# Kernel tuning notes

Hardware: AMD Instinct MI355X
Metric: run time of the kernel (lower is better)

The kernel has to match this reference:

```python
import jax, jax.numpy as jnp
import numpy as np

HID, NHEAD, NLAYERS = 128, 8, 6
BS, H, W = 1, 64, 128
HD = HID // NHEAD  # head dim = 16


def layer_norm(x, g, b, eps=1e-5):
    m = jnp.mean(x, -1, keepdims=True)
    v = jnp.mean((x - m) ** 2, -1, keepdims=True)
    return (x - m) * jax.lax.rsqrt(v + eps) * g + b


def mha_relative(query, kv, in_w, in_b, out_w, out_b, pos_enc, pos_idx, attn_mask, is_self):
    # query/kv: [W, N, C]; in_w: [3C, C]; pos_enc: [2W-1, C]; pos_idx: [W*W]
    w, n, c = query.shape
    if is_self:
        q, k, v = jnp.split(query @ in_w.T + in_b, 3, axis=-1)
    else:
        q = query @ in_w[:c].T + in_b[:c]
        k, v = jnp.split(kv @ in_w[c:].T + in_b[c:], 2, axis=-1)
    # relative positional bias: gather [2W-1,C] -> [W,W,C], project with q/k weights
    pos_sel = pos_enc[pos_idx].reshape(w, w, c)
    q_r, k_r = jnp.split(pos_sel @ in_w[:2 * c].T + in_b[:2 * c], 2, axis=-1)
    scale = HD ** -0.5
    q = (q * scale).reshape(w, n, NHEAD, HD)
    k = k.reshape(w, n, NHEAD, HD)
    v = v.reshape(w, n, NHEAD, HD)
    q_r = (q_r * scale).reshape(w, w, NHEAD, HD)
    k_r = k_r.reshape(w, w, NHEAD, HD)
    attn = (jnp.einsum('wnec,vnec->newv', q, k)
            + jnp.einsum('wnec,wvec->newv', q, k_r)
            + jnp.einsum('vnec,wvec->newv', k, q_r))  # [N,E,W,W]
    if attn_mask is not None:
        attn = attn + attn_mask[None, None]
    raw_attn = attn.sum(axis=1)  # [N,W,W] head-summed raw scores
    a = jax.nn.softmax(attn, axis=-1)
    v_o = jnp.einsum('newv,vnec->wnec', a, v).reshape(w, n, c)
    return v_o @ out_w.T + out_b, raw_attn


def setup_inputs() -> dict:
    key = jax.random.key(0)
    ks = jax.random.split(key, 8)
    f32 = jnp.float32
    s = 0.02
    d = {}
    d['feat_left'] = jax.random.normal(ks[0], (BS, HID, H, W), f32)
    d['feat_right'] = jax.random.normal(ks[1], (BS, HID, H, W), f32)
    d['pos_enc'] = jax.random.normal(ks[2], (2 * W - 1, HID), f32)
    d['self_ln_g'] = jnp.ones((NLAYERS, HID), f32)
    d['self_ln_b'] = jnp.zeros((NLAYERS, HID), f32)
    d['self_in_w'] = jax.random.normal(ks[3], (NLAYERS, 3 * HID, HID), f32) * s
    d['self_in_b'] = jnp.zeros((NLAYERS, 3 * HID), f32)
    d['self_out_w'] = jax.random.normal(ks[4], (NLAYERS, HID, HID), f32) * s
    d['self_out_b'] = jnp.zeros((NLAYERS, HID), f32)
    d['cross_ln1_g'] = jnp.ones((NLAYERS, HID), f32)
    d['cross_ln1_b'] = jnp.zeros((NLAYERS, HID), f32)
    d['cross_ln2_g'] = jnp.ones((NLAYERS, HID), f32)
    d['cross_ln2_b'] = jnp.zeros((NLAYERS, HID), f32)
    d['cross_in_w'] = jax.random.normal(ks[5], (NLAYERS, 3 * HID, HID), f32) * s
    d['cross_in_b'] = jnp.zeros((NLAYERS, 3 * HID), f32)
    d['cross_out_w'] = jax.random.normal(ks[6], (NLAYERS, HID, HID), f32) * s
    d['cross_out_b'] = jnp.zeros((NLAYERS, HID), f32)
    return d


def reference(feat_left, feat_right, pos_enc, self_ln_g, self_ln_b, self_in_w, self_in_b,
              self_out_w, self_out_b, cross_ln1_g, cross_ln1_b, cross_ln2_g, cross_ln2_b,
              cross_in_w, cross_in_b, cross_out_w, cross_out_b):
    bs, c, hn, w = feat_left.shape  # bs must be 1 (as in source)
    # [N,C,H,W] -> [W, H*N, C]
    fl = jnp.transpose(feat_left, (3, 2, 0, 1)).reshape(w, hn * bs, c)
    fr = jnp.transpose(feat_right, (3, 2, 0, 1)).reshape(w, hn * bs, c)
    HN = hn * bs
    # pos_indexes[i,j] = (w-1-i) + j, values in [0, 2w-2]
    pos_idx = ((w - 1 - jnp.arange(w))[:, None] + jnp.arange(w)[None, :]).reshape(-1)
    causal = jnp.triu(jnp.full((w, w), -jnp.inf, feat_left.dtype), k=1)
    feat = jnp.concatenate([fl, fr], axis=1)  # [W, 2HN, C]
    raw_attn = None
    for i in range(NLAYERS):
        # self attention over concatenated left+right rows
        f2 = layer_norm(feat, self_ln_g[i], self_ln_b[i])
        upd, _ = mha_relative(f2, f2, self_in_w[i], self_in_b[i], self_out_w[i],
                              self_out_b[i], pos_enc, pos_idx, None, True)
        feat = feat + upd
        left, right = feat[:, :HN], feat[:, HN:]
        # cross attention: left queries attend to norm2(right)
        # (source computes a right-update with norm1/flipped pos but discards it)
        l2 = layer_norm(left, cross_ln1_g[i], cross_ln1_b[i])
        r2 = layer_norm(right, cross_ln2_g[i], cross_ln2_b[i])
        mask = causal if i == NLAYERS - 1 else None
        upd, raw_attn = mha_relative(l2, r2, cross_in_w[i], cross_in_b[i], cross_out_w[i],
                                     cross_out_b[i], pos_enc, pos_idx, mask, False)
        left = left + upd
        feat = jnp.concatenate([left, right], axis=1)
    # [HN,W,W] -> [bs, hn, W, W]
    return jnp.transpose(raw_attn.reshape(hn, bs, w, w), (1, 0, 2, 3))
```

## Files before the change

kernel.cpp:

```cpp
#include <hip/hip_runtime.h>
#include <cmath>

#define CDIM 128

typedef __attribute__((ext_vector_type(8))) short bf16x8;
typedef __attribute__((ext_vector_type(4))) float f32x4;
typedef unsigned short u16;

__device__ inline unsigned pk2(float a, float b) {
    unsigned ua = __float_as_uint(a) + 0x8000u;
    unsigned ub = __float_as_uint(b) + 0x8000u;
    return (ua >> 16) | (ub & 0xffff0000u);
}
__device__ inline u16 pk1(float x) {
    return (u16)((__float_as_uint(x) + 0x8000u) >> 16);
}
__device__ inline float ubf(u16 u) { return __uint_as_float(((unsigned)u) << 16); }
__device__ inline float ulo(unsigned u) { return __uint_as_float(u << 16); }
__device__ inline float uhi(unsigned u) { return __uint_as_float(u & 0xffff0000u); }

__global__ __launch_bounds__(256) void init_feat_kernel(const float* __restrict__ FL,
                                                        const float* __restrict__ FR,
                                                        u16* __restrict__ feat) {
    __shared__ float t[32][33];
    int cb = blockIdx.x, wb = blockIdx.y, n = blockIdx.z;
    const float* src = (n < 64) ? FL : FR;
    int nn = n & 63;
    int j = threadIdx.x & 31, i0 = threadIdx.x >> 5;
    #pragma unroll
    for (int p = 0; p < 4; p++) {
        int i = i0 + p * 8;
        t[i][j] = src[(cb * 32 + i) * 8192 + nn * 128 + wb * 32 + j];
    }
    __syncthreads();
    #pragma unroll
    for (int p = 0; p < 4; p++) {
        int i = i0 + p * 8;
        feat[((long)(wb * 32 + i) * 128 + n) * 128 + cb * 32 + j] = pk1(t[j][i]);
    }
}

__global__ __launch_bounds__(256) void convert_w_kernel(const float* __restrict__ w0,
                                                        const float* __restrict__ w1,
                                                        const float* __restrict__ w2,
                                                        const float* __restrict__ w3,
                                                        const float* __restrict__ b0,
                                                        const float* __restrict__ b1,
                                                        u16* __restrict__ wout,
                                                        float* __restrict__ bout) {
    int idx = blockIdx.x * 256 + threadIdx.x;
    if (idx < 196608) {
        const float* src; long off4; u16* dst;
        if (idx < 73728)       { src = w0; off4 = idx;           dst = wout; }
        else if (idx < 147456) { src = w1; off4 = idx - 73728;   dst = wout + 294912; }
        else if (idx < 172032) { src = w2; off4 = idx - 147456;  dst = wout + 589824; }
        else                   { src = w3; off4 = idx - 172032;  dst = wout + 688128; }
        float4 f = *(const float4*)(src + off4 * 4);
        *(uint2*)(dst + off4 * 4) = make_uint2(pk2(f.x, f.y), pk2(f.z, f.w));
    } else {
        int t = idx - 196608;
        if (t < 4608) bout[t] = (t < 2304) ? b0[t] : b1[t - 2304];
    }
}

__global__ __launch_bounds__(256) void ln0_kernel(const u16* __restrict__ feat,
                                                  const float* __restrict__ g,
                                                  const float* __restrict__ b,
                                                  u16* __restrict__ lnB) {
    int tid = threadIdx.x, wv = tid >> 6, lane = tid & 63;
    float g0 = g[lane * 2], b0 = b[lane * 2];
    float g1 = g[lane * 2 + 1], b1 = b[lane * 2 + 1];
    #pragma unroll
    for (int rr = 0; rr < 4; rr++) {
        long m = (long)blockIdx.x * 16 + wv * 4 + rr;
        unsigned u = *(const unsigned*)(feat + m * 128 + lane * 2);
        float x0 = ulo(u), x1 = uhi(u);
        float s = x0 + x1, q = x0 * x0 + x1 * x1;
        #pragma unroll
        for (int off = 1; off < 64; off <<= 1) {
            s += __shfl_xor(s, off);
            q += __shfl_xor(q, off);
        }
        float mean = s * (1.f / 128.f);
        float var = q * (1.f / 128.f) - mean * mean;
        float rs = rsqrtf(var + 1e-5f);
        float y0 = (x0 - mean) * rs * g0 + b0;
        float y1 = (x1 - mean) * rs * g1 + b1;
        *(unsigned*)(lnB + m * 128 + lane * 2) = pk2(y0, y1);
    }
}

__global__ __launch_bounds__(256, 4) void gemm_pp_kernel(const float* __restrict__ A,
                                                         const u16* __restrict__ W,
                                                         const float* __restrict__ bias,
                                                         u16* __restrict__ C,
                                                         int M, int N, int ldc,
                                                         float scale,
                                                         int wz, int bz, int cz) {
    __shared__ __align__(16) u16 sA[64 * 136];
    __shared__ __align__(16) u16 sW[64 * 136];
    int z = blockIdx.z;
    W += (long)z * wz;
    bias += z * bz;
    C += (long)z * cz;
    int tid = threadIdx.x;
    int row0 = blockIdx.y * 64, col0 = blockIdx.x * 64;
    float4 zf4 = make_float4(0.f, 0.f, 0.f, 0.f);
    int kc = tid & 31;
    #pragma unroll
    for (int i = 0; i < 8; i++) {
        int r = (tid + i * 256) >> 5;
        int m = row0 + r;
        int jn = col0 + r;
        float4 fa = (m < M) ? *(const float4*)(A + (long)m * 128 + kc * 4) : zf4;
        uint2 uw = make_uint2(0u, 0u);
        if (jn < N) uw = *(const uint2*)(W + (long)jn * 128 + kc * 4);
        *(uint2*)&sA[r * 136 + kc * 4] = make_uint2(pk2(fa.x, fa.y), pk2(fa.z, fa.w));
        *(uint2*)&sW[r * 136 + kc * 4] = uw;
    }
    __syncthreads();

    int wv = tid >> 6, lane = tid & 63, quad = lane >> 4, col = lane & 15;
    f32x4 z4 = {0.f, 0.f, 0.f, 0.f};
    f32x4 acc0 = z4, acc1 = z4, acc2 = z4, acc3 = z4;
    #pragma unroll
    for (int kb = 0; kb < 4; kb++) {
        bf16x8 a = *(const bf16x8*)&sA[(wv * 16 + col) * 136 + kb * 32 + quad * 8];
        bf16x8 b0 = *(const bf16x8*)&sW[(0 * 16 + col) * 136 + kb * 32 + quad * 8];
        bf16x8 b1 = *(const bf16x8*)&sW[(1 * 16 + col) * 136 + kb * 32 + quad * 8];
        bf16x8 b2 = *(const bf16x8*)&sW[(2 * 16 + col) * 136 + kb * 32 + quad * 8];
        bf16x8 b3 = *(const bf16x8*)&sW[(3 * 16 + col) * 136 + kb * 32 + quad * 8];
        acc0 = __builtin_amdgcn_mfma_f32_16x16x32_bf16(a, b0, acc0, 0, 0, 0);
        acc1 = __builtin_amdgcn_mfma_f32_16x16x32_bf16(a, b1, acc1, 0, 0, 0);
        acc2 = __builtin_amdgcn_mfma_f32_16x16x32_bf16(a, b2, acc2, 0, 0, 0);
        acc3 = __builtin_amdgcn_mfma_f32_16x16x32_bf16(a, b3, acc3, 0, 0, 0);
    }
    int mrow = row0 + wv * 16 + quad * 4;
    #pragma unroll
    for (int tc = 0; tc < 4; tc++) {
        f32x4 acc = tc == 0 ? acc0 : tc == 1 ? acc1 : tc == 2 ? acc2 : acc3;
        int jn = col0 + tc * 16 + col;
        if (jn >= N) continue;
        float bs = bias[jn];
        float sc = (jn < 128) ? scale : 1.f;
        #pragma unroll
        for (int reg = 0; reg < 4; reg++) {
            int m = mrow + reg;
            if (m >= M) continue;
            C[(long)m * ldc + jn] = pk1((acc[reg] + bs) * sc);
        }
    }
}

__global__ __launch_bounds__(256, 3) void gemm_qkv128_kernel(const u16* __restrict__ A,
                                                             const u16* __restrict__ W,
                                                             const float* __restrict__ bias,
                                                             u16* __restrict__ C,
                                                             float scale) {
    __shared__ __align__(16) u16 sA[128 * 136];
    __shared__ __align__(16) u16 sW[64 * 136];
    int tid = threadIdx.x;
    int row0 = blockIdx.y * 128, col0 = blockIdx.x * 64;
    int kc = tid & 31;
    #pragma unroll
    for (int i = 0; i < 16; i++) {
        int r = (tid + i * 256) >> 5;
        *(uint2*)&sA[r * 136 + kc * 4] =
            *(const uint2*)(A + (long)(row0 + r) * 128 + kc * 4);
    }
    #pragma unroll
    for (int i = 0; i < 8; i++) {
        int r = (tid + i * 256) >> 5;
        *(uint2*)&sW[r * 136 + kc * 4] =
            *(const uint2*)(W + (long)(col0 + r) * 128 + kc * 4);
    }
    __syncthreads();

    int wv = tid >> 6, lane = tid & 63, quad = lane >> 4, col = lane & 15;
    f32x4 z4 = {0.f, 0.f, 0.f, 0.f};
    f32x4 accA0 = z4, accA1 = z4, accA2 = z4, accA3 = z4;
    f32x4 accB0 = z4, accB1 = z4, accB2 = z4, accB3 = z4;
    #pragma unroll
    for (int kb = 0; kb < 4; kb++) {
        bf16x8 a0 = *(const bf16x8*)&sA[(wv * 32 + col) * 136 + kb * 32 + quad * 8];
        bf16x8 a1 = *(const bf16x8*)&sA[(wv * 32 + 16 + col) * 136 + kb * 32 + quad * 8];
        bf16x8 b0 = *(const bf16x8*)&sW[(0 * 16 + col) * 136 + kb * 32 + quad * 8];
        bf16x8 b1 = *(const bf16x8*)&sW[(1 * 16 + col) * 136 + kb * 32 + quad * 8];
        bf16x8 b2 = *(const bf16x8*)&sW[(2 * 16 + col) * 136 + kb * 32 + quad * 8];
        bf16x8 b3 = *(const bf16x8*)&sW[(3 * 16 + col) * 136 + kb * 32 + quad * 8];
        accA0 = __builtin_amdgcn_mfma_f32_16x16x32_bf16(a0, b0, accA0, 0, 0, 0);
        accA1 = __builtin_amdgcn_mfma_f32_16x16x32_bf16(a0, b1, accA1, 0, 0, 0);
        accA2 = __builtin_amdgcn_mfma_f32_16x16x32_bf16(a0, b2, accA2, 0, 0, 0);
        accA3 = __builtin_amdgcn_mfma_f32_16x16x32_bf16(a0, b3, accA3, 0, 0, 0);
        accB0 = __builtin_amdgcn_mfma_f32_16x16x32_bf16(a1, b0, accB0, 0, 0, 0);
        accB1 = __builtin_amdgcn_mfma_f32_16x16x32_bf16(a1, b1, accB1, 0, 0, 0);
        accB2 = __builtin_amdgcn_mfma_f32_16x16x32_bf16(a1, b2, accB2, 0, 0, 0);
        accB3 = __builtin_amdgcn_mfma_f32_16x16x32_bf16(a1, b3, accB3, 0, 0, 0);
    }
    #pragma unroll
    for (int st = 0; st < 2; st++) {
        int mrow = row0 + wv * 32 + st * 16 + quad * 4;
        #pragma unroll
        for (int tc = 0; tc < 4; tc++) {
            f32x4 acc;
            if (st == 0) acc = tc == 0 ? accA0 : tc == 1 ? accA1 : tc == 2 ? accA2 : accA3;
            else         acc = tc == 0 ? accB0 : tc == 1 ? accB1 : tc == 2 ? accB2 : accB3;
            int jn = col0 + tc * 16 + col;
            float bs = bias[jn];
            float sc = (jn < 128) ? scale : 1.f;
            #pragma unroll
            for (int reg = 0; reg < 4; reg++)
                C[(long)(mrow + reg) * 384 + jn] = pk1((acc[reg] + bs) * sc);
        }
    }
}

__global__ __launch_bounds__(256, 3) void gemm_out_self_kernel(const u16* __restrict__ A,
                                                               const u16* __restrict__ W,
                                                               const float* __restrict__ bias,
                                                               u16* __restrict__ feat,
                                                               const float* __restrict__ g1,
                                                               const float* __restrict__ b1,
                                                               const float* __restrict__ g2,
                                                               const float* __restrict__ b2,
                                                               u16* __restrict__ lnA,
                                                               const float* __restrict__ sng,
                                                               const float* __restrict__ snb,
                                                               u16* __restrict__ lnB) {
    __shared__ __align__(16) u16 sA[64 * 136];
    __shared__ __align__(16) u16 sW[128 * 136];
    int tid = threadIdx.x;
    int by = blockIdx.x;
    int row0 = by * 64;
    int kc = tid & 31;
    #pragma unroll
    for (int i = 0; i < 8; i++) {
        int r = (tid + i * 256) >> 5;
        *(uint2*)&sA[r * 136 + kc * 4] = *(const uint2*)(A + (long)(row0 + r) * 128 + kc * 4);
    }
    #pragma unroll
    for (int i = 0; i < 16; i++) {
        int r = (tid + i * 256) >> 5;
        *(uint2*)&sW[r * 136 + kc * 4] = *(const uint2*)(W + (long)r * 128 + kc * 4);
    }
    __syncthreads();

    int wv = tid >> 6, lane = tid & 63, quad = lane >> 4, col = lane & 15;
    f32x4 acc[8] = {};
    #pragma unroll
    for (int kb = 0; kb < 4; kb++) {
        bf16x8 a = *(const bf16x8*)&sA[(wv * 16 + col) * 136 + kb * 32 + quad * 8];
        #pragma unroll
        for (int tc = 0; tc < 8; tc++) {
            bf16x8 b = *(const bf16x8*)&sW[(tc * 16 + col) * 136 + kb * 32 + quad * 8];
            acc[tc] = __builtin_amdgcn_mfma_f32_16x16x32_bf16(a, b, acc[tc], 0, 0, 0);
        }
    }
    int right = by & 1;
    const float* gA = right ? g2 : g1;
    const float* bA = right ? b2 : b1;
    float gAv[8], bAv[8], gBv[8], bBv[8], bsv[8];
    bool doB = (sng != nullptr) && right;
    #pragma unroll
    for (int tc = 0; tc < 8; tc++) {
        int jn = tc * 16 + col;
        gAv[tc] = gA[jn]; bAv[tc] = bA[jn]; bsv[tc] = bias[jn];
        if (doB) { gBv[tc] = sng[jn]; bBv[tc] = snb[jn]; }
    }
    #pragma unroll
    for (int reg = 0; reg < 4; reg++) {
        long m = row0 + wv * 16 + quad * 4 + reg;
        long rb = m * 128;
        float o[8];
        float s = 0.f, q = 0.f;
        #pragma unroll
        for (int tc = 0; tc < 8; tc++) {
            int jn = tc * 16 + col;
            float v = acc[tc][reg] + bsv[tc] + ubf(feat[rb + jn]);
            o[tc] = v; s += v; q += v * v;
        }
        #pragma unroll
        for (int off = 1; off < 16; off <<= 1) {
            s += __shfl_xor(s, off);
            q += __shfl_xor(q, off);
        }
        float mean = s * (1.f / 128.f);
        float var = q * (1.f / 128.f) - mean * mean;
        float rs = rsqrtf(var + 1e-5f);
        #pragma unroll
        for (int tc = 0; tc < 8; tc++) {
            int jn = tc * 16 + col;
            feat[rb + jn] = pk1(o[tc]);
            float ln = (o[tc] - mean) * rs;
            lnA[rb + jn] = pk1(ln * gAv[tc] + bAv[tc]);
            if (doB) lnB[rb + jn] = pk1(ln * gBv[tc] + bBv[tc]);
        }
    }
}

__global__ __launch_bounds__(256, 3) void gemm_out_cross_kernel(const u16* __restrict__ A,
                                                                const u16* __restrict__ W,
                                                                const float* __restrict__ bias,
                                                                u16* __restrict__ feat,
                                                                const float* __restrict__ sng,
                                                                const float* __restrict__ snb,
                                                                u16* __restrict__ lnB) {
    __shared__ __align__(16) u16 sA[64 * 136];
    __shared__ __align__(16) u16 sW[128 * 136];
    int tid = threadIdx.x;
    int row0 = blockIdx.x * 64;
    int kc = tid & 31;
    #pragma unroll
    for (int i = 0; i < 8; i++) {
        int r = (tid + i * 256) >> 5;
        *(uint2*)&sA[r * 136 + kc * 4] = *(const uint2*)(A + (long)(row0 + r) * 128 + kc * 4);
    }
    #pragma unroll
    for (int i = 0; i < 16; i++) {
        int r = (tid + i * 256) >> 5;
        *(uint2*)&sW[r * 136 + kc * 4] = *(const uint2*)(W + (long)r * 128 + kc * 4);
    }
    __syncthreads();

    int wv = tid >> 6, lane = tid & 63, quad = lane >> 4, col = lane & 15;
    f32x4 acc[8] = {};
    #pragma unroll
    for (int kb = 0; kb < 4; kb++) {
        bf16x8 a = *(const bf16x8*)&sA[(wv * 16 + col) * 136 + kb * 32 + quad * 8];
        #pragma unroll
        for (int tc = 0; tc < 8; tc++) {
            bf16x8 b = *(const bf16x8*)&sW[(tc * 16 + col) * 136 + kb * 32 + quad * 8];
            acc[tc] = __builtin_amdgcn_mfma_f32_16x16x32_bf16(a, b, acc[tc], 0, 0, 0);
        }
    }
    float gBv[8], bBv[8], bsv[8];
    #pragma unroll
    for (int tc = 0; tc < 8; tc++) {
        int jn = tc * 16 + col;
        gBv[tc] = sng[jn]; bBv[tc] = snb[jn]; bsv[tc] = bias[jn];
    }
    #pragma unroll
    for (int reg = 0; reg < 4; reg++) {
        long m = row0 + wv * 16 + quad * 4 + reg;
        long rb = ((m >> 6) * 128 + (m & 63)) * 128;
        float o[8];
        float s = 0.f, q = 0.f;
        #pragma unroll
        for (int tc = 0; tc < 8; tc++) {
            int jn = tc * 16 + col;
            float v = acc[tc][reg] + bsv[tc] + ubf(feat[rb + jn]);
            o[tc] = v; s += v; q += v * v;
        }
        #pragma unroll
        for (int off = 1; off < 16; off <<= 1) {
            s += __shfl_xor(s, off);
            q += __shfl_xor(q, off);
        }
        float mean = s * (1.f / 128.f);
        float var = q * (1.f / 128.f) - mean * mean;
        float rs = rsqrtf(var + 1e-5f);
        #pragma unroll
        for (int tc = 0; tc < 8; tc++) {
            int jn = tc * 16 + col;
            feat[rb + jn] = pk1(o[tc]);
            lnB[rb + jn] = pk1((o[tc] - mean) * rs * gBv[tc] + bBv[tc]);
        }
    }
}

__global__ __launch_bounds__(256, 4) void gemm_cross_qkv_kernel(const u16* __restrict__ lnA,
                                                                const u16* __restrict__ Wq,
                                                                const float* __restrict__ biasq,
                                                                u16* __restrict__ qout,
                                                                u16* __restrict__ kvout,
                                                                float scale) {
    int bx = blockIdx.x;
    int z = (bx >= 2) ? 1 : 0;
    int cx = z ? bx - 2 : bx;
    const u16* W     = z ? Wq + 16384 : Wq;
    const float* bia = z ? biasq + 128 : biasq;
    u16* C           = z ? kvout : qout;
    int N   = z ? 256 : 128;
    int ldc = N;
    int n_off = z ? 64 : 0;
    float sc  = z ? 1.f : scale;

    __shared__ __align__(16) u16 sA[64 * 136];
    __shared__ __align__(16) u16 sW[64 * 136];
    int tid = threadIdx.x;
    int row0 = blockIdx.y * 64, col0 = cx * 64;
    int kc = tid & 31;
    #pragma unroll
    for (int i = 0; i < 8; i++) {
        int r = (tid + i * 256) >> 5;
        int m = row0 + r;
        int jn = col0 + r;
        long xr = (long)((m >> 6) * 128 + (m & 63) + n_off);
        uint2 uw = make_uint2(0u, 0u);
        if (jn < N) uw = *(const uint2*)(W + (long)jn * 128 + kc * 4);
        *(uint2*)&sA[r * 136 + kc * 4] = *(const uint2*)(lnA + xr * 128 + kc * 4);
        *(uint2*)&sW[r * 136 + kc * 4] = uw;
    }
    __syncthreads();

    int wv = tid >> 6, lane = tid & 63, quad = lane >> 4, col = lane & 15;
    f32x4 z4 = {0.f, 0.f, 0.f, 0.f};
    f32x4 acc0 = z4, acc1 = z4, acc2 = z4, acc3 = z4;
    #pragma unroll
    for (int kb = 0; kb < 4; kb++) {
        bf16x8 a = *(const bf16x8*)&sA[(wv * 16 + col) * 136 + kb * 32 + quad * 8];
        bf16x8 b0 = *(const bf16x8*)&sW[(0 * 16 + col) * 136 + kb * 32 + quad * 8];
        bf16x8 b1 = *(const bf16x8*)&sW[(1 * 16 + col) * 136 + kb * 32 + quad * 8];
        bf16x8 b2 = *(const bf16x8*)&sW[(2 * 16 + col) * 136 + kb * 32 + quad * 8];
        bf16x8 b3 = *(const bf16x8*)&sW[(3 * 16 + col) * 136 + kb * 32 + quad * 8];
        acc0 = __builtin_amdgcn_mfma_f32_16x16x32_bf16(a, b0, acc0, 0, 0, 0);
        acc1 = __builtin_amdgcn_mfma_f32_16x16x32_bf16(a, b1, acc1, 0, 0, 0);
        acc2 = __builtin_amdgcn_mfma_f32_16x16x32_bf16(a, b2, acc2, 0, 0, 0);
        acc3 = __builtin_amdgcn_mfma_f32_16x16x32_bf16(a, b3, acc3, 0, 0, 0);
    }
    int mrow = row0 + wv * 16 + quad * 4;
    #pragma unroll
    for (int tc = 0; tc < 4; tc++) {
        f32x4 acc = tc == 0 ? acc0 : tc == 1 ? acc1 : tc == 2 ? acc2 : acc3;
        int jn = col0 + tc * 16 + col;
        if (jn >= N) continue;
        float bs = bia[jn];
        #pragma unroll
        for (int reg = 0; reg < 4; reg++) {
            int m = mrow + reg;
            C[(long)m * ldc + jn] = pk1((acc[reg] + bs) * sc);
        }
    }
}

__global__ __launch_bounds__(512, 6) void attn_kernel(const u16* __restrict__ Q, int qs,
                                                      const u16* __restrict__ K, int ks,
                                                      const u16* __restrict__ V, int vs,
                                                      const u16* __restrict__ PP,
                                                      u16* __restrict__ VO,
                                                      float* __restrict__ RAW,
                                                      int NN, int causal) {
    __shared__ __align__(16) u16 sm[26624];
    const int SK = 0, R2 = 3072, SA = 9216;
    int e = blockIdx.x, n = blockIdx.y;
    int tid = threadIdx.x;
    int wv = tid >> 6, lane = tid & 63, quad = lane >> 4, col = lane & 15;

    bf16x8 zf = {0, 0, 0, 0, 0, 0, 0, 0};
    f32x4 z4 = {0.f, 0.f, 0.f, 0.f};
    bf16x8 aQ = zf, aK = zf;
    if (quad < 2) {
        aQ = *(const bf16x8*)(Q + (long)((wv * 16 + col) * NN + n) * qs + e * 16 + quad * 8);
        aK = *(const bf16x8*)(K + (long)((wv * 16 + col) * NN + n) * ks + e * 16 + quad * 8);
    }
    {
        int row = tid >> 2, c = tid & 3;
        *(uint2*)&sm[SK + row * 24 + c * 4] =
            *(const uint2*)(K + (long)(row * NN + n) * ks + e * 16 + c * 4);
    }
    for (int t = tid; t < 1024; t += 512) {
        int r = t >> 2, c = t & 3;
        uint2 uk = make_uint2(0u, 0u);
        if (r < 255) uk = *(const uint2*)(PP + r * 256 + 128 + e * 16 + c * 4);
        *(uint2*)&sm[R2 + r * 24 + c * 4] = uk;
    }
    __syncthreads();

    f32x4 s1[8];
    #pragma unroll
    for (int tv = 0; tv < 8; tv++) {
        bf16x8 b = zf;
        if (quad < 2) b = *(const bf16x8*)&sm[SK + (tv * 16 + col) * 24 + quad * 8];
        s1[tv] = __builtin_amdgcn_mfma_f32_16x16x32_bf16(aQ, b, z4, 0, 0, 0);
    }
    int wbq = wv * 16 + quad * 4;
    int s2lo = 7 - wv;
    for (int tt = 0; tt < 9; tt++) {
        int tr = s2lo + tt;
        bf16x8 b = zf;
        if (quad < 2) b = *(const bf16x8*)&sm[R2 + (tr * 16 + col) * 24 + quad * 8];
        f32x4 d = __builtin_amdgcn_mfma_f32_16x16x32_bf16(aQ, b, z4, 0, 0, 0);
        #pragma unroll
        for (int reg = 0; reg < 4; reg++) {
            int v = tr * 16 + col - 127 + wbq + reg;
            if (v >= 0 && v < 128) sm[SA + (wbq + reg) * 136 + v] = pk1(d[reg]);
        }
    }
    __syncthreads();
    for (int t = tid; t < 1024; t += 512) {
        int r = t >> 2, c = t & 3;
        uint2 uq = make_uint2(0u, 0u);
        if (r < 255) uq = *(const uint2*)(PP + r * 256 + e * 16 + c * 4);
        *(uint2*)&sm[R2 + r * 24 + c * 4] = uq;
    }
    {
        int row = tid >> 2, c = tid & 3;
        uint2 uv = *(const uint2*)(V + (long)(row * NN + n) * vs + e * 16 + c * 4);
        sm[SK + (c * 4 + 0) * 136 + row] = (u16)(uv.x & 0xffffu);
        sm[SK + (c * 4 + 1) * 136 + row] = (u16)(uv.x >> 16);
        sm[SK + (c * 4 + 2) * 136 + row] = (u16)(uv.y & 0xffffu);
        sm[SK + (c * 4 + 3) * 136 + row] = (u16)(uv.y >> 16);
    }
    __syncthreads();
    for (int tt = 0; tt < 9; tt++) {
        int tr = wv + tt;
        bf16x8 b = zf;
        if (quad < 2) b = *(const bf16x8*)&sm[R2 + (tr * 16 + col) * 24 + quad * 8];
        f32x4 d = __builtin_amdgcn_mfma_f32_16x16x32_bf16(aK, b, z4, 0, 0, 0);
        #pragma unroll
        for (int reg = 0; reg < 4; reg++) {
            int v = wbq + reg;
            int w = 127 + v - (tr * 16 + col);
            if (w >= 0 && w < 128) {
                int addr = SA + w * 136 + v;
                sm[addr] = pk1(ubf(sm[addr]) + d[reg]);
            }
        }
    }
    __syncthreads();

    float rs0 = 0.f, rs1 = 0.f, rs2 = 0.f, rs3 = 0.f;
    #pragma unroll
    for (int tv = 0; tv < 8; tv++) {
        f32x4 c = s1[tv];
        int v = tv * 16 + col;
        #pragma unroll
        for (int reg = 0; reg < 4; reg++) {
            int w = wbq + reg;
            int addr = SA + w * 136 + v;
            float a = c[reg] + ubf(sm[addr]);
            bool live = !(causal && v > w);
            float p = live ? __expf(a) : 0.f;
            if (RAW) RAW[(long)n * 16384 + w * 128 + v] = live ? a : 0.f;
            sm[addr] = pk1(p);
            if (reg == 0) rs0 += p; else if (reg == 1) rs1 += p;
            else if (reg == 2) rs2 += p; else rs3 += p;
        }
    }
    #pragma unroll
    for (int o = 1; o < 16; o <<= 1) {
        rs0 += __shfl_xor(rs0, o);
        rs1 += __shfl_xor(rs1, o);
        rs2 += __shfl_xor(rs2, o);
        rs3 += __shfl_xor(rs3, o);
    }
    __syncthreads();

    f32x4 o4 = z4;
    #pragma unroll
    for (int kb = 0; kb < 4; kb++) {
        bf16x8 a = *(const bf16x8*)&sm[SA + (wv * 16 + col) * 136 + kb * 32 + quad * 8];
        bf16x8 b = *(const bf16x8*)&sm[SK + col * 136 + kb * 32 + quad * 8];
        o4 = __builtin_amdgcn_mfma_f32_16x16x32_bf16(a, b, o4, 0, 0, 0);
    }
    float iv0 = 1.f / rs0, iv1 = 1.f / rs1, iv2 = 1.f / rs2, iv3 = 1.f / rs3;
    VO[(long)((wbq + 0) * NN + n) * CDIM + e * 16 + col] = pk1(o4[0] * iv0);
    VO[(long)((wbq + 1) * NN + n) * CDIM + e * 16 + col] = pk1(o4[1] * iv1);
    VO[(long)((wbq + 2) * NN + n) * CDIM + e * 16 + col] = pk1(o4[2] * iv2);
    VO[(long)((wbq + 3) * NN + n) * CDIM + e * 16 + col] = pk1(o4[3] * iv3);
}

extern "C" void kernel_launch(void* const* d_in, const int* in_sizes, int n_in,
                              void* d_out, int out_size, void* d_ws, size_t ws_size,
                              hipStream_t stream) {
    const float* FL         = (const float*)d_in[0];
    const float* FR         = (const float*)d_in[1];
    const float* pos_enc    = (const float*)d_in[2];
    const float* self_ln_g  = (const float*)d_in[3];
    const float* self_ln_b  = (const float*)d_in[4];
    const float* self_in_w  = (const float*)d_in[5];
    const float* self_in_b  = (const float*)d_in[6];
    const float* self_out_w = (const float*)d_in[7];
    const float* self_out_b = (const float*)d_in[8];
    const float* cr_ln1_g   = (const float*)d_in[9];
    const float* cr_ln1_b   = (const float*)d_in[10];
    const float* cr_ln2_g   = (const float*)d_in[11];
    const float* cr_ln2_b   = (const float*)d_in[12];
    const float* cr_in_w    = (const float*)d_in[13];
    const float* cr_in_b    = (const float*)d_in[14];
    const float* cr_out_w   = (const float*)d_in[15];
    const float* cr_out_b   = (const float*)d_in[16];

    float* ws       = (float*)d_ws;
    u16*   feat     = (u16*)ws;
    u16*   vo       = (u16*)(ws + 1048576);
    u16*   qkv      = (u16*)(ws + 2097152);
    u16*   kvx      = qkv + 3145728;
    u16*   pp_self  = (u16*)(ws + 5242880);
    u16*   pp_cross = pp_self + 391680;
    u16*   wbf      = (u16*)(ws + 5634560);
    u16*   wsel_in  = wbf;
    u16*   wcr_in   = wbf + 294912;
    u16*   wsel_out = wbf + 589824;
    u16*   wcr_out  = wbf + 688128;
    float* bin      = ws + 6027776;
    u16*   lnA      = (u16*)(ws + 6032384);
    u16*   lnB      = (u16*)(ws + 7080960);
    float* out      = (float*)d_out;

    const float scale = 0.25f;

    convert_w_kernel<<<786, 256, 0, stream>>>(self_in_w, cr_in_w, self_out_w, cr_out_w,
                                              self_in_b, cr_in_b, wbf, bin);
    init_feat_kernel<<<dim3(4, 4, 128), 256, 0, stream>>>(FL, FR, feat);
    ln0_kernel<<<1024, 256, 0, stream>>>(feat, self_ln_g, self_ln_b, lnB);
    gemm_pp_kernel<<<dim3(4, 4, 12), 256, 0, stream>>>(pos_enc, wsel_in, bin, pp_self,
                                                       255, 256, 256, scale,
                                                       49152, 384, 65280);

    for (int i = 0; i < 6; i++) {
        int last = (i == 5);
        gemm_qkv128_kernel<<<dim3(6, 128), 256, 0, stream>>>(lnB, wsel_in + i * 49152,
                                                             self_in_b + i * 384, qkv, scale);
        attn_kernel<<<dim3(8, 128), 512, 0, stream>>>(qkv, 384, qkv + 128, 384, qkv + 256, 384,
                                                      pp_self + i * 65280, vo, nullptr, 128, 0);
        gemm_out_self_kernel<<<256, 256, 0, stream>>>(vo, wsel_out + i * 16384,
                                                      self_out_b + i * 128, feat,
                                                      cr_ln1_g + i * 128, cr_ln1_b + i * 128,
                                                      cr_ln2_g + i * 128, cr_ln2_b + i * 128,
                                                      lnA,
                                                      last ? nullptr : self_ln_g + (i + 1) * 128,
                                                      last ? nullptr : self_ln_b + (i + 1) * 128,
                                                      lnB);

        gemm_cross_qkv_kernel<<<dim3(6, 128), 256, 0, stream>>>(lnA, wcr_in + i * 49152,
                                                                cr_in_b + i * 384,
                                                                qkv, kvx, scale);
        attn_kernel<<<dim3(8, 64), 512, 0, stream>>>(qkv, 128,
                                                     kvx, 256,
                                                     kvx + 128, 256,
                                                     pp_cross + i * 65280, vo,
                                                     last ? out : nullptr,
                                                     64, last);
        if (!last) {
            gemm_out_cross_kernel<<<128, 256, 0, stream>>>(vo, wcr_out + i * 16384,
                                                           cr_out_b + i * 128, feat,
                                                           self_ln_g + (i + 1) * 128,
                                                           self_ln_b + (i + 1) * 128,
                                                           lnB);
        }
    }
}
```

Before: 545.5 us.

## Store QKV and positional projections in head-major contiguous layout for attention

The QKV projection GEMMs (self and cross) and the positional-projection GEMM now write their outputs head-major, as [head][n][w][16] and [head][r][16]. The attention kernel can then read each head's Q/K/V and relative-position rows as contiguous 32-byte rows instead of strided gathers across 384/256-wide rows. This improves coalescing of the attention loads. The cost is more scattered 2-byte stores in the GEMM epilogues, and separate kvx buffer handling is dropped in favour of one shared buffer.

After: 531.2 us. -2.6%, faster.

```diff
diff --git a/kernel.cpp b/kernel.cpp
--- a/kernel.cpp
+++ b/kernel.cpp
@@ -94,7 +94,7 @@
                                                          const u16* __restrict__ W,
                                                          const float* __restrict__ bias,
                                                          u16* __restrict__ C,
-                                                         int M, int N, int ldc,
+                                                         int M, int N,
                                                          float scale,
                                                          int wz, int bz, int cz) {
     __shared__ __align__(16) u16 sA[64 * 136];
@@ -143,11 +143,12 @@
         if (jn >= N) continue;
         float bs = bias[jn];
         float sc = (jn < 128) ? scale : 1.f;
+        long db = ((long)(jn >> 4) * 255) * 16 + (jn & 15);
         #pragma unroll
         for (int reg = 0; reg < 4; reg++) {
             int m = mrow + reg;
             if (m >= M) continue;
-            C[(long)m * ldc + jn] = pk1((acc[reg] + bs) * sc);
+            C[db + (long)m * 16] = pk1((acc[reg] + bs) * sc);
         }
     }
 }
@@ -197,9 +198,10 @@
         accB2 = __builtin_amdgcn_mfma_f32_16x16x32_bf16(a1, b2, accB2, 0, 0, 0);
         accB3 = __builtin_amdgcn_mfma_f32_16x16x32_bf16(a1, b3, accB3, 0, 0, 0);
     }
+    long woff = (long)blockIdx.y * 16;
     #pragma unroll
     for (int st = 0; st < 2; st++) {
-        int mrow = row0 + wv * 32 + st * 16 + quad * 4;
+        int nrow = wv * 32 + st * 16 + quad * 4;
         #pragma unroll
         for (int tc = 0; tc < 4; tc++) {
             f32x4 acc;
@@ -208,9 +210,10 @@
             int jn = col0 + tc * 16 + col;
             float bs = bias[jn];
             float sc = (jn < 128) ? scale : 1.f;
+            long db = ((long)(jn >> 4) * 128) * 2048 + woff + (jn & 15);
             #pragma unroll
             for (int reg = 0; reg < 4; reg++)
-                C[(long)(mrow + reg) * 384 + jn] = pk1((acc[reg] + bs) * sc);
+                C[db + (long)(nrow + reg) * 2048] = pk1((acc[reg] + bs) * sc);
         }
     }
 }
@@ -371,19 +374,16 @@
 __global__ __launch_bounds__(256, 4) void gemm_cross_qkv_kernel(const u16* __restrict__ lnA,
                                                                 const u16* __restrict__ Wq,
                                                                 const float* __restrict__ biasq,
-                                                                u16* __restrict__ qout,
-                                                                u16* __restrict__ kvout,
+                                                                u16* __restrict__ QKV,
                                                                 float scale) {
     int bx = blockIdx.x;
     int z = (bx >= 2) ? 1 : 0;
     int cx = z ? bx - 2 : bx;
     const u16* W     = z ? Wq + 16384 : Wq;
     const float* bia = z ? biasq + 128 : biasq;
-    u16* C           = z ? kvout : qout;
-    int N   = z ? 256 : 128;
-    int ldc = N;
     int n_off = z ? 64 : 0;
     float sc  = z ? 1.f : scale;
+    int N = z ? 256 : 128;
 
     __shared__ __align__(16) u16 sA[64 * 136];
     __shared__ __align__(16) u16 sW[64 * 136];
@@ -418,25 +418,24 @@
         acc2 = __builtin_amdgcn_mfma_f32_16x16x32_bf16(a, b2, acc2, 0, 0, 0);
         acc3 = __builtin_amdgcn_mfma_f32_16x16x32_bf16(a, b3, acc3, 0, 0, 0);
     }
-    int mrow = row0 + wv * 16 + quad * 4;
+    long woff = (long)blockIdx.y * 16;
+    int sadd = z ? 8 : 0;
     #pragma unroll
     for (int tc = 0; tc < 4; tc++) {
         f32x4 acc = tc == 0 ? acc0 : tc == 1 ? acc1 : tc == 2 ? acc2 : acc3;
         int jn = col0 + tc * 16 + col;
         if (jn >= N) continue;
         float bs = bia[jn];
-        #pragma unroll
-        for (int reg = 0; reg < 4; reg++) {
-            int m = mrow + reg;
-            C[(long)m * ldc + jn] = pk1((acc[reg] + bs) * sc);
-        }
-    }
-}
-
-__global__ __launch_bounds__(512, 6) void attn_kernel(const u16* __restrict__ Q, int qs,
-                                                      const u16* __restrict__ K, int ks,
-                                                      const u16* __restrict__ V, int vs,
-                                                      const u16* __restrict__ PP,
+        long db = ((long)((jn >> 4) + sadd) * 64) * 2048 + woff + (jn & 15);
+        int nrow = wv * 16 + quad * 4;
+        #pragma unroll
+        for (int reg = 0; reg < 4; reg++)
+            QKV[db + (long)(nrow + reg) * 2048] = pk1((acc[reg] + bs) * sc);
+    }
+}
+
+__global__ __launch_bounds__(512, 6) void attn_kernel(const u16* __restrict__ QKV,
+                                                      const u16* __restrict__ PPL,
                                                       u16* __restrict__ VO,
                                                       float* __restrict__ RAW,
                                                       int NN, int causal) {
@@ -446,22 +445,27 @@
     int tid = threadIdx.x;
     int wv = tid >> 6, lane = tid & 63, quad = lane >> 4, col = lane & 15;
 
+    const u16* qb = QKV + ((long)e * NN + n) * 2048;
+    const u16* kb = QKV + ((long)(8 + e) * NN + n) * 2048;
+    const u16* vb = QKV + ((long)(16 + e) * NN + n) * 2048;
+    const u16* qr = PPL + (long)e * 4080;
+    const u16* kr = PPL + (long)(8 + e) * 4080;
+
     bf16x8 zf = {0, 0, 0, 0, 0, 0, 0, 0};
     f32x4 z4 = {0.f, 0.f, 0.f, 0.f};
     bf16x8 aQ = zf, aK = zf;
     if (quad < 2) {
-        aQ = *(const bf16x8*)(Q + (long)((wv * 16 + col) * NN + n) * qs + e * 16 + quad * 8);
-        aK = *(const bf16x8*)(K + (long)((wv * 16 + col) * NN + n) * ks + e * 16 + quad * 8);
+        aQ = *(const bf16x8*)(qb + (wv * 16 + col) * 16 + quad * 8);
+        aK = *(const bf16x8*)(kb + (wv * 16 + col) * 16 + quad * 8);
     }
     {
         int row = tid >> 2, c = tid & 3;
-        *(uint2*)&sm[SK + row * 24 + c * 4] =
-            *(const uint2*)(K + (long)(row * NN + n) * ks + e * 16 + c * 4);
+        *(uint2*)&sm[SK + row * 24 + c * 4] = *(const uint2*)(kb + row * 16 + c * 4);
     }
     for (int t = tid; t < 1024; t += 512) {
         int r = t >> 2, c = t & 3;
         uint2 uk = make_uint2(0u, 0u);
-        if (r < 255) uk = *(const uint2*)(PP + r * 256 + 128 + e * 16 + c * 4);
+        if (r < 255) uk = *(const uint2*)(kr + r * 16 + c * 4);
         *(uint2*)&sm[R2 + r * 24 + c * 4] = uk;
     }
     __syncthreads();
@@ -490,12 +494,12 @@
     for (int t = tid; t < 1024; t += 512) {
         int r = t >> 2, c = t & 3;
         uint2 uq = make_uint2(0u, 0u);
-        if (r < 255) uq = *(const uint2*)(PP + r * 256 + e * 16 + c * 4);
+        if (r < 255) uq = *(const uint2*)(qr + r * 16 + c * 4);
         *(uint2*)&sm[R2 + r * 24 + c * 4] = uq;
     }
     {
         int row = tid >> 2, c = tid & 3;
-        uint2 uv = *(const uint2*)(V + (long)(row * NN + n) * vs + e * 16 + c * 4);
+        uint2 uv = *(const uint2*)(vb + row * 16 + c * 4);
         sm[SK + (c * 4 + 0) * 136 + row] = (u16)(uv.x & 0xffffu);
         sm[SK + (c * 4 + 1) * 136 + row] = (u16)(uv.x >> 16);
         sm[SK + (c * 4 + 2) * 136 + row] = (u16)(uv.y & 0xffffu);
@@ -584,8 +588,7 @@
     float* ws       = (float*)d_ws;
     u16*   feat     = (u16*)ws;
     u16*   vo       = (u16*)(ws + 1048576);
-    u16*   qkv      = (u16*)(ws + 2097152);
-    u16*   kvx      = qkv + 3145728;
+    u16*   qkvS     = (u16*)(ws + 2097152);
     u16*   pp_self  = (u16*)(ws + 5242880);
     u16*   pp_cross = pp_self + 391680;
     u16*   wbf      = (u16*)(ws + 5634560);
@@ -605,15 +608,15 @@
     init_feat_kernel<<<dim3(4, 4, 128), 256, 0, stream>>>(FL, FR, feat);
     ln0_kernel<<<1024, 256, 0, stream>>>(feat, self_ln_g, self_ln_b, lnB);
     gemm_pp_kernel<<<dim3(4, 4, 12), 256, 0, stream>>>(pos_enc, wsel_in, bin, pp_self,
-                                                       255, 256, 256, scale,
+                                                       255, 256, scale,
                                                        49152, 384, 65280);
 
     for (int i = 0; i < 6; i++) {
         int last = (i == 5);
         gemm_qkv128_kernel<<<dim3(6, 128), 256, 0, stream>>>(lnB, wsel_in + i * 49152,
-                                                             self_in_b + i * 384, qkv, scale);
-        attn_kernel<<<dim3(8, 128), 512, 0, stream>>>(qkv, 384, qkv + 128, 384, qkv + 256, 384,
-                                                      pp_self + i * 65280, vo, nullptr, 128, 0);
+                                                             self_in_b + i * 384, qkvS, scale);
+        attn_kernel<<<dim3(8, 128), 512, 0, stream>>>(qkvS, pp_self + i * 65280,
+                                                      vo, nullptr, 128, 0);
         gemm_out_self_kernel<<<256, 256, 0, stream>>>(vo, wsel_out + i * 16384,
                                                       self_out_b + i * 128, feat,
                                                       cr_ln1_g + i * 128, cr_ln1_b + i * 128,
@@ -625,12 +628,9 @@
 
         gemm_cross_qkv_kernel<<<dim3(6, 128), 256, 0, stream>>>(lnA, wcr_in + i * 49152,
                                                                 cr_in_b + i * 384,
-                                                                qkv, kvx, scale);
-        attn_kernel<<<dim3(8, 64), 512, 0, stream>>>(qkv, 128,
-                                                     kvx, 256,
-                                                     kvx + 128, 256,
-                                                     pp_cross + i * 65280, vo,
-                                                     last ? out : nullptr,
+                                                                qkvS, scale);
+        attn_kernel<<<dim3(8, 64), 512, 0, stream>>>(qkvS, pp_cross + i * 65280,
+                                                     vo, last ? out : nullptr,
                                                      64, last);
         if (!last) {
             gemm_out_cross_kernel<<<128, 256, 0, stream>>>(vo, wcr_out + i * 16384,
```
